# Kernel tuning notes

Measured on AMD Instinct MI355X. Metric: run time of the kernel, lower is better.

Reference implementation:

```python
import jax, jax.numpy as jnp
import numpy as np

BLOCK_LEN = 64

def _segsum(x):
    # x: (..., T) -> (..., T, T) with entry [t, s] = sum_{u=s+1..t} x[u], -inf above diagonal
    T = x.shape[-1]
    cs = jnp.cumsum(x, axis=-1)
    ss = cs[..., :, None] - cs[..., None, :]
    mask = jnp.tril(jnp.ones((T, T), dtype=bool))
    return jnp.where(mask, ss, -jnp.inf)

def setup_inputs() -> dict:
    key = jax.random.key(0)
    kx, ka, kb, kc = jax.random.split(key, 4)
    b, L, h, p, n = 4, 4096, 32, 64, 16
    X = jax.random.normal(kx, (b, L, h, p), dtype=jnp.float32)
    # negative, small-magnitude A so exp(cumsum(A)) stays finite (decaying SSM),
    # matching the math of the module while keeping the baseline numerically sane
    A = -0.1 * jnp.abs(jax.random.normal(ka, (b, L, h), dtype=jnp.float32))
    B = jax.random.normal(kb, (b, L, h, n), dtype=jnp.float32)
    C = jax.random.normal(kc, (b, L, h, n), dtype=jnp.float32)
    return {"X": X, "A": A, "B": B, "C": C}

def reference(X, A, B, C):
    b, L, h, p = X.shape
    n = B.shape[-1]
    l = BLOCK_LEN
    c = L // l
    # chunk into blocks
    Xb = X.reshape(b, c, l, h, p)                       # b c l h p
    Ab = A.reshape(b, c, l, h).transpose(0, 3, 1, 2)    # b h c l
    Bb = B.reshape(b, c, l, h, n)                       # b c l h n
    Cb = C.reshape(b, c, l, h, n)                       # b c l h n
    A_cumsum = jnp.cumsum(Ab, axis=-1)                  # b h c l
    # intra-chunk (diagonal) term; equals the fused per-timestep scan
    # h_t = exp(A_t)*h_{t-1} + B_t*x_t ; y_t = C_t . h_t
    Lmat = jnp.exp(_segsum(Ab))                         # b h c l l (lower-tri)
    Y_diag = jnp.einsum('bclhn,bcshn,bhcls,bcshp->bclhp', Cb, Bb, Lmat, Xb)
    # per-chunk end states
    decay_states = jnp.exp(A_cumsum[..., -1:] - A_cumsum)  # b h c l
    states = jnp.einsum('bclhn,bhcl,bclhp->bchpn', Bb, decay_states, Xb)
    states = jnp.concatenate([jnp.zeros_like(states[:, :1]), states], axis=1)  # b (c+1) h p n
    # inter-chunk recurrence via segment-sum of chunk totals
    decay_chunk = jnp.exp(_segsum(jnp.pad(A_cumsum[..., -1], ((0, 0), (0, 0), (1, 0)))))  # b h (c+1) (c+1)
    new_states = jnp.einsum('bhzc,bchpn->bzhpn', decay_chunk, states)
    states = new_states[:, :-1]                          # b c h p n
    # state -> output contribution
    state_decay_out = jnp.exp(A_cumsum)                  # b h c l
    Y_off = jnp.einsum('bclhn,bchpn,bhcl->bclhp', Cb, states, state_decay_out)
    return (Y_diag + Y_off).reshape(b, L, h, p)
```

## Files before the change

### kernel.cpp

```cpp
#include <hip/hip_runtime.h>

#define BATCH   4
#define SEQLEN  4096
#define NHEADS  32
#define PDIM    64
#define NDIM    16
#define CHUNK   64
#define NCHUNK  64
#define PHALF   32

typedef short v8s __attribute__((ext_vector_type(8)));
typedef float v4f __attribute__((ext_vector_type(4)));

union V8U { v8s s; unsigned u[4]; };

__device__ __forceinline__ short f2bf(float f) {
    union { float f; unsigned u; } x; x.f = f;
    unsigned r = (x.u + 0x7FFFu + ((x.u >> 16) & 1u)) >> 16;
    return (short)r;
}
__device__ __forceinline__ float bf2f(short s) {
    union { unsigned u; float f; } x; x.u = ((unsigned)(unsigned short)s) << 16;
    return x.f;
}
__device__ __forceinline__ unsigned cvt_pk_bf16(float lo, float hi) {
    unsigned r;
    asm("v_cvt_pk_bf16_f32 %0, %1, %2" : "=v"(r) : "v"(lo), "v"(hi));
    return r;
}

__device__ __forceinline__ float wave_iscan(float v, int lane) {
#pragma unroll
    for (int d = 1; d < 64; d <<= 1) {
        float o = __shfl_up(v, (unsigned)d, 64);
        if (lane >= d) v += o;
    }
    return v;
}

__global__ __launch_bounds__(512) void k_fused(
    const float* __restrict__ X, const float* __restrict__ A,
    const float* __restrict__ Bm, const float* __restrict__ Cm,
    float* __restrict__ Y)
{
    const int ph = blockIdx.x, hh = blockIdx.y, bb = blockIdx.z;
    const int tid = threadIdx.x;
    const int lane = tid & 63;
    const int wv = tid >> 6;
    const int W = wv & 3;
    const int qq = lane >> 4, nn = lane & 15;

    __shared__ __align__(16) float sCumAll[SEQLEN];
    __shared__ __align__(16) short xF [4][4][64][8];
    __shared__ __align__(16) short xSF[4][4][64][8];
    __shared__ __align__(16) short cFq[4][2048];
    __shared__ __align__(16) short bFq[4][2048];
    __shared__ __align__(16) short bFs[4][1024];
    __shared__ __align__(16) short sF [4][1024];
    __shared__ __align__(16) float gRawA[CHUNK][68];
    __shared__ __align__(16) float gRawB[CHUNK][68];
    __shared__ float wtot[8];

    {
        const v8s z8 = {0,0,0,0,0,0,0,0};
        ((v8s*)cFq)[tid] = z8; ((v8s*)cFq)[tid + 512] = z8;
        ((v8s*)bFq)[tid] = z8; ((v8s*)bFq)[tid + 512] = z8;
        if (tid < 128) ((v8s*)sF)[tid] = z8;
    }

    {
        const float* Ab = A + (size_t)bb * SEQLEN * NHEADS + hh;
        const int tb = wv * 512 + lane * 8;
        float av[8];
#pragma unroll
        for (int j = 0; j < 8; ++j) av[j] = Ab[(size_t)(tb + j) * NHEADS];
        float s8 = 0.f;
#pragma unroll
        for (int j = 0; j < 8; ++j) s8 += av[j];
        const float pre = wave_iscan(s8, lane);
        if (lane == 63) wtot[wv] = pre;
        __syncthreads();
        float base = 0.f;
#pragma unroll
        for (int w = 0; w < 7; ++w) if (w < wv) base += wtot[w];
        float c = base + pre - s8;
#pragma unroll
        for (int j = 0; j < 8; ++j) { c += av[j]; sCumAll[tb + j] = c; }
        __syncthreads();
    }

    auto stage = [&](int c, int buf) {
        const int t0c = bb * SEQLEN + c * CHUNK;
        const float* gcc = &sCumAll[c * CHUNK];
        const int ti = wv - 4, kk = ti >> 1, nt = ti & 1;
        const int trow = kk * 32 + qq * 8;
        const float* xb = X + ((size_t)(t0c + trow) * NHEADS + hh) * PDIM
                            + ph * PHALF + nt * 16 + nn;
        float xv[8];
#pragma unroll
        for (int j = 0; j < 8; ++j) xv[j] = xb[(size_t)j * (NHEADS * PDIM)];
        const float gtot = gcc[63];
        float ex[8];
#pragma unroll
        for (int j = 0; j < 8; ++j) ex[j] = __expf(gtot - gcc[trow + j]);
        V8U xf, xs;
#pragma unroll
        for (int j2 = 0; j2 < 4; ++j2) {
            xf.u[j2] = cvt_pk_bf16(xv[2*j2], xv[2*j2+1]);
            xs.u[j2] = cvt_pk_bf16(xv[2*j2] * ex[2*j2], xv[2*j2+1] * ex[2*j2+1]);
        }
        *(v8s*)&xF [buf][kk*2+nt][lane][0] = xf.s;
        *(v8s*)&xSF[buf][kk*2+nt][lane][0] = xs.s;
        const int ptid = tid & 255;
        const int r = ptid >> 2, n0 = (ptid & 3) * 4;
        const float4 bv = *(const float4*)&Bm[((size_t)(t0c + r) * NHEADS + hh) * NDIM + n0];
        const int offq = ((r >> 4) * 64 + (n0 >> 3) * 16 + (r & 15)) * 8 + (n0 & 7);
        bFq[buf][offq + 0] = f2bf(bv.x); bFq[buf][offq + 1] = f2bf(bv.y);
        bFq[buf][offq + 2] = f2bf(bv.z); bFq[buf][offq + 3] = f2bf(bv.w);
        const int kb = r >> 5, qb = (r >> 3) & 3, jj = r & 7;
        const int bs = (kb * 64 + qb * 16) * 8 + jj;
        bFs[buf][bs + (n0 + 0) * 8] = f2bf(bv.x);
        bFs[buf][bs + (n0 + 1) * 8] = f2bf(bv.y);
        bFs[buf][bs + (n0 + 2) * 8] = f2bf(bv.z);
        bFs[buf][bs + (n0 + 3) * 8] = f2bf(bv.w);
        const float4 cv = *(const float4*)&Cm[((size_t)(t0c + r) * NHEADS + hh) * NDIM + n0];
        cFq[buf][offq + 0] = f2bf(cv.x); cFq[buf][offq + 1] = f2bf(cv.y);
        cFq[buf][offq + 2] = f2bf(cv.z); cFq[buf][offq + 3] = f2bf(cv.w);
    };

    const v4f zero = {0.f, 0.f, 0.f, 0.f};

    auto qk_g = [&](float (*gR)[68], const float* gc, int buf, int tau) -> v8s {
        const v8s cfrag = *(const v8s*)&cFq[buf][(tau * 64 + lane) * 8];
        float tc[4];
#pragma unroll
        for (int r = 0; r < 4; ++r) tc[r] = gc[tau * 16 + qq * 4 + r];
#pragma unroll
        for (int st = 0; st < 4; ++st) {
            if (st <= tau) {
                const v8s bfrag = *(const v8s*)&bFq[buf][(st * 64 + lane) * 8];
                v4f acc = __builtin_amdgcn_mfma_f32_16x16x32_bf16(cfrag, bfrag, zero, 0, 0, 0);
                const float cums = gc[st * 16 + nn];
#pragma unroll
                for (int r = 0; r < 4; ++r) {
                    const int t = tau * 16 + qq * 4 + r;
                    const int s = st * 16 + nn;
                    gR[t][s] = (t >= s) ? acc[r] * __expf(tc[r] - cums) : 0.f;
                }
            }
        }
        if (tau == 0) {
#pragma unroll
            for (int r = 0; r < 4; ++r) gR[qq * 4 + r][16 + nn] = 0.f;
        } else if (tau == 2) {
#pragma unroll
            for (int r = 0; r < 4; ++r) gR[32 + qq * 4 + r][48 + nn] = 0.f;
        }
        return cfrag;
    };

    auto do_y = [&](float (*gR)[68], const float* gc, float gbase, int buf,
                    int t0c, v8s cfrag) {
        const float et = __expf(gc[W * 16 + nn] - gbase);
        V8U cef;
#pragma unroll
        for (int j2 = 0; j2 < 4; ++j2)
            cef.u[j2] = cvt_pk_bf16(bf2f(cfrag[2*j2]) * et, bf2f(cfrag[2*j2+1]) * et);
        V8U ga0u, ga1u;
        {
            const float* gr = &gR[W * 16 + nn][qq * 8];
#pragma unroll
            for (int j2 = 0; j2 < 4; ++j2) ga0u.u[j2] = cvt_pk_bf16(gr[2*j2], gr[2*j2+1]);
        }
        const bool usekk1 = (W >= 2);
        if (usekk1) {
            const float* gr = &gR[W * 16 + nn][32 + qq * 8];
#pragma unroll
            for (int j2 = 0; j2 < 4; ++j2) ga1u.u[j2] = cvt_pk_bf16(gr[2*j2], gr[2*j2+1]);
        }
        v4f ya[2];
#pragma unroll
        for (int nt2 = 0; nt2 < 2; ++nt2) {
            const v8s sfrag = *(const v8s*)&sF[buf][(nt2 * 64 + lane) * 8];
            v4f a = __builtin_amdgcn_mfma_f32_16x16x32_bf16(cef.s, sfrag, zero, 0, 0, 0);
            const v8s x0 = *(const v8s*)&xF[buf][0 + nt2][lane][0];
            a = __builtin_amdgcn_mfma_f32_16x16x32_bf16(ga0u.s, x0, a, 0, 0, 0);
            if (usekk1) {
                const v8s x1 = *(const v8s*)&xF[buf][2 + nt2][lane][0];
                a = __builtin_amdgcn_mfma_f32_16x16x32_bf16(ga1u.s, x1, a, 0, 0, 0);
            }
            ya[nt2] = a;
        }
#pragma unroll
        for (int r = 0; r < 4; ++r) {
            const int t = W * 16 + qq * 4 + r;
            float* yp = Y + ((size_t)(t0c + t) * NHEADS + hh) * PDIM + ph * PHALF + nn;
            yp[0]  = ya[0][r];
            yp[16] = ya[1][r];
        }
    };

    auto do_state = [&](int buf, float Et, int pub, v4f& S) {
        const v8s a0 = *(const v8s*)&xSF[buf][0 + W][lane][0];
        const v8s a1 = *(const v8s*)&xSF[buf][2 + W][lane][0];
        const v8s b0 = *(const v8s*)&bFs[buf][(0 * 64 + lane) * 8];
        const v8s b1 = *(const v8s*)&bFs[buf][(1 * 64 + lane) * 8];
        v4f sa = __builtin_amdgcn_mfma_f32_16x16x32_bf16(a0, b0, zero, 0, 0, 0);
        sa = __builtin_amdgcn_mfma_f32_16x16x32_bf16(a1, b1, sa, 0, 0, 0);
#pragma unroll
        for (int r = 0; r < 4; ++r) S[r] = Et * S[r] + sa[r];
        short* d = &sF[pub][0];
#pragma unroll
        for (int r = 0; r < 4; ++r)
            d[(W * 64 + (nn >> 3) * 16 + qq * 4 + r) * 8 + (nn & 7)] = f2bf(S[r]);
    };

    if (wv >= 4) { stage(0, 0); stage(1, 1); }
    __syncthreads();

    v4f S = {0.f, 0.f, 0.f, 0.f};
    v8s cfragB = {0,0,0,0,0,0,0,0};

#pragma unroll 1
    for (int k = 0; k < NCHUNK; k += 2) {
        const int bufA = k & 3, bufB = (k + 1) & 3;
        const float* gcA = &sCumAll[k * CHUNK];
        const float* gcB = gcA + CHUNK;

        if (wv >= 4) {
            if (k + 2 < NCHUNK) stage(k + 2, (k + 2) & 3);
        } else {
            __builtin_amdgcn_s_setprio(1);
            const float gbaseA = (k == 0) ? 0.f : gcA[-1];
            const int t0cA = bb * SEQLEN + k * CHUNK;
            const v8s cfragA = qk_g(gRawA, gcA, bufA, W);
            qk_g(gRawB, gcB, bufB, 3 - W);
            do_y(gRawA, gcA, gbaseA, bufA, t0cA, cfragA);
            if (W < 2) {
                do_state(bufA, __expf(gcA[63] - gbaseA), bufB, S);
                do_state(bufB, __expf(gcB[63] - gcA[63]), (k + 2) & 3, S);
            }
            __builtin_amdgcn_s_setprio(0);
        }
        __syncthreads();

        if (wv >= 4) {
            if (k + 3 < NCHUNK) stage(k + 3, (k + 3) & 3);
        } else {
            __builtin_amdgcn_s_setprio(1);
            const int t0cB = bb * SEQLEN + (k + 1) * CHUNK;
            cfragB = *(const v8s*)&cFq[bufB][(W * 64 + lane) * 8];
            do_y(gRawB, gcB, gcA[63], bufB, t0cB, cfragB);
            __builtin_amdgcn_s_setprio(0);
        }
        __syncthreads();
    }
}

extern "C" void kernel_launch(void* const* d_in, const int* in_sizes, int n_in,
                              void* d_out, int out_size, void* d_ws, size_t ws_size,
                              hipStream_t stream) {
    const float* X  = (const float*)d_in[0];
    const float* A  = (const float*)d_in[1];
    const float* Bm = (const float*)d_in[2];
    const float* Cm = (const float*)d_in[3];
    float* Y = (float*)d_out;
    (void)d_ws; (void)ws_size;

    dim3 grid(2, NHEADS, BATCH);
    k_fused<<<grid, 512, 0, stream>>>(X, A, Bm, Cm, Y);
}
```

Baseline: 308.3 us.

## Process one chunk per iteration and move state recurrence to producer waves

```diff
diff --git a/kernel.cpp b/kernel.cpp
--- a/kernel.cpp
+++ b/kernel.cpp
@@ -57,8 +57,7 @@
     __shared__ __align__(16) short bFq[4][2048];
     __shared__ __align__(16) short bFs[4][1024];
     __shared__ __align__(16) short sF [4][1024];
-    __shared__ __align__(16) float gRawA[CHUNK][68];
-    __shared__ __align__(16) float gRawB[CHUNK][68];
+    __shared__ __align__(16) float gRaw[CHUNK][68];
     __shared__ float wtot[8];
 
     {
@@ -130,37 +129,36 @@
 
     const v4f zero = {0.f, 0.f, 0.f, 0.f};
 
-    auto qk_g = [&](float (*gR)[68], const float* gc, int buf, int tau) -> v8s {
-        const v8s cfrag = *(const v8s*)&cFq[buf][(tau * 64 + lane) * 8];
+    auto qk_g = [&](const float* gc, int buf) -> v8s {
+        const v8s cfrag = *(const v8s*)&cFq[buf][(W * 64 + lane) * 8];
         float tc[4];
 #pragma unroll
-        for (int r = 0; r < 4; ++r) tc[r] = gc[tau * 16 + qq * 4 + r];
+        for (int r = 0; r < 4; ++r) tc[r] = gc[W * 16 + qq * 4 + r];
 #pragma unroll
         for (int st = 0; st < 4; ++st) {
-            if (st <= tau) {
+            if (st <= W) {
                 const v8s bfrag = *(const v8s*)&bFq[buf][(st * 64 + lane) * 8];
                 v4f acc = __builtin_amdgcn_mfma_f32_16x16x32_bf16(cfrag, bfrag, zero, 0, 0, 0);
                 const float cums = gc[st * 16 + nn];
 #pragma unroll
                 for (int r = 0; r < 4; ++r) {
-                    const int t = tau * 16 + qq * 4 + r;
+                    const int t = W * 16 + qq * 4 + r;
                     const int s = st * 16 + nn;
-                    gR[t][s] = (t >= s) ? acc[r] * __expf(tc[r] - cums) : 0.f;
+                    gRaw[t][s] = (t >= s) ? acc[r] * __expf(tc[r] - cums) : 0.f;
                 }
             }
         }
-        if (tau == 0) {
-#pragma unroll
-            for (int r = 0; r < 4; ++r) gR[qq * 4 + r][16 + nn] = 0.f;
-        } else if (tau == 2) {
-#pragma unroll
-            for (int r = 0; r < 4; ++r) gR[32 + qq * 4 + r][48 + nn] = 0.f;
+        if (W == 0) {
+#pragma unroll
+            for (int r = 0; r < 4; ++r) gRaw[qq * 4 + r][16 + nn] = 0.f;
+        } else if (W == 2) {
+#pragma unroll
+            for (int r = 0; r < 4; ++r) gRaw[32 + qq * 4 + r][48 + nn] = 0.f;
         }
         return cfrag;
     };
 
-    auto do_y = [&](float (*gR)[68], const float* gc, float gbase, int buf,
-                    int t0c, v8s cfrag) {
+    auto do_y = [&](const float* gc, float gbase, int buf, int t0c, v8s cfrag) {
         const float et = __expf(gc[W * 16 + nn] - gbase);
         V8U cef;
 #pragma unroll
@@ -168,13 +166,13 @@
             cef.u[j2] = cvt_pk_bf16(bf2f(cfrag[2*j2]) * et, bf2f(cfrag[2*j2+1]) * et);
         V8U ga0u, ga1u;
         {
-            const float* gr = &gR[W * 16 + nn][qq * 8];
+            const float* gr = &gRaw[W * 16 + nn][qq * 8];
 #pragma unroll
             for (int j2 = 0; j2 < 4; ++j2) ga0u.u[j2] = cvt_pk_bf16(gr[2*j2], gr[2*j2+1]);
         }
         const bool usekk1 = (W >= 2);
         if (usekk1) {
-            const float* gr = &gR[W * 16 + nn][32 + qq * 8];
+            const float* gr = &gRaw[W * 16 + nn][32 + qq * 8];
 #pragma unroll
             for (int j2 = 0; j2 < 4; ++j2) ga1u.u[j2] = cvt_pk_bf16(gr[2*j2], gr[2*j2+1]);
         }
@@ -200,57 +198,40 @@
         }
     };
 
-    auto do_state = [&](int buf, float Et, int pub, v4f& S) {
-        const v8s a0 = *(const v8s*)&xSF[buf][0 + W][lane][0];
-        const v8s a1 = *(const v8s*)&xSF[buf][2 + W][lane][0];
-        const v8s b0 = *(const v8s*)&bFs[buf][(0 * 64 + lane) * 8];
-        const v8s b1 = *(const v8s*)&bFs[buf][(1 * 64 + lane) * 8];
-        v4f sa = __builtin_amdgcn_mfma_f32_16x16x32_bf16(a0, b0, zero, 0, 0, 0);
-        sa = __builtin_amdgcn_mfma_f32_16x16x32_bf16(a1, b1, sa, 0, 0, 0);
-#pragma unroll
-        for (int r = 0; r < 4; ++r) S[r] = Et * S[r] + sa[r];
-        short* d = &sF[pub][0];
-#pragma unroll
-        for (int r = 0; r < 4; ++r)
-            d[(W * 64 + (nn >> 3) * 16 + qq * 4 + r) * 8 + (nn & 7)] = f2bf(S[r]);
-    };
-
     if (wv >= 4) { stage(0, 0); stage(1, 1); }
     __syncthreads();
 
     v4f S = {0.f, 0.f, 0.f, 0.f};
-    v8s cfragB = {0,0,0,0,0,0,0,0};
 
 #pragma unroll 1
-    for (int k = 0; k < NCHUNK; k += 2) {
-        const int bufA = k & 3, bufB = (k + 1) & 3;
-        const float* gcA = &sCumAll[k * CHUNK];
-        const float* gcB = gcA + CHUNK;
+    for (int k = 0; k < NCHUNK; ++k) {
+        const int buf = k & 3;
+        const float* gc = &sCumAll[k * CHUNK];
+        const float gbase = (k == 0) ? 0.f : gc[-1];
 
         if (wv >= 4) {
             if (k + 2 < NCHUNK) stage(k + 2, (k + 2) & 3);
+            if (wv < 6) {
+                const int Wp = wv - 4;
+                const v8s a0 = *(const v8s*)&xSF[buf][0 + Wp][lane][0];
+                const v8s a1 = *(const v8s*)&xSF[buf][2 + Wp][lane][0];
+                const v8s b0 = *(const v8s*)&bFs[buf][(0 * 64 + lane) * 8];
+                const v8s b1 = *(const v8s*)&bFs[buf][(1 * 64 + lane) * 8];
+                v4f sa = __builtin_amdgcn_mfma_f32_16x16x32_bf16(a0, b0, zero, 0, 0, 0);
+                sa = __builtin_amdgcn_mfma_f32_16x16x32_bf16(a1, b1, sa, 0, 0, 0);
+                const float Et = __expf(gc[63] - gbase);
+#pragma unroll
+                for (int r = 0; r < 4; ++r) S[r] = Et * S[r] + sa[r];
+                short* d = &sF[(k + 1) & 3][0];
+#pragma unroll
+                for (int r = 0; r < 4; ++r)
+                    d[(Wp * 64 + (nn >> 3) * 16 + qq * 4 + r) * 8 + (nn & 7)] = f2bf(S[r]);
+            }
         } else {
             __builtin_amdgcn_s_setprio(1);
-            const float gbaseA = (k == 0) ? 0.f : gcA[-1];
-            const int t0cA = bb * SEQLEN + k * CHUNK;
-            const v8s cfragA = qk_g(gRawA, gcA, bufA, W);
-            qk_g(gRawB, gcB, bufB, 3 - W);
-            do_y(gRawA, gcA, gbaseA, bufA, t0cA, cfragA);
-            if (W < 2) {
-                do_state(bufA, __expf(gcA[63] - gbaseA), bufB, S);
-                do_state(bufB, __expf(gcB[63] - gcA[63]), (k + 2) & 3, S);
-            }
-            __builtin_amdgcn_s_setprio(0);
-        }
-        __syncthreads();
-
-        if (wv >= 4) {
-            if (k + 3 < NCHUNK) stage(k + 3, (k + 3) & 3);
-        } else {
-            __builtin_amdgcn_s_setprio(1);
-            const int t0cB = bb * SEQLEN + (k + 1) * CHUNK;
-            cfragB = *(const v8s*)&cFq[bufB][(W * 64 + lane) * 8];
-            do_y(gRawB, gcB, gcA[63], bufB, t0cB, cfragB);
+            const int t0c = bb * SEQLEN + k * CHUNK;
+            const v8s cfrag = qk_g(gc, buf);
+            do_y(gc, gbase, buf, t0c, cfrag);
             __builtin_amdgcn_s_setprio(0);
         }
         __syncthreads();
```

New measurement: 313.7 us. About the same (+1.8%).
